# Optimization experiments

Measured on AMD Instinct MI355X. Metric: run time of the kernel, lower is better.

## Reference

```python
import jax, jax.numpy as jnp
import numpy as np

B, D, H, OUT = 16384, 4096, 7, 7


def setup_inputs() -> dict:
    key = jax.random.key(0)
    k1, k2, k3, k4 = jax.random.split(key, 4)
    features1 = jax.random.normal(k1, (B, D), dtype=jnp.float32)
    features2 = jax.random.normal(k2, (B, D), dtype=jnp.float32)
    W1 = jax.random.normal(k3, (D, H), dtype=jnp.float32) * (1.0 / np.sqrt(D))
    b1 = jnp.zeros((H,), dtype=jnp.float32)
    W2 = jax.random.normal(k4, (H, OUT), dtype=jnp.float32) * (1.0 / np.sqrt(H))
    b2 = jnp.zeros((OUT,), dtype=jnp.float32)
    return {"features1": features1, "features2": features2,
            "W1": W1, "b1": b1, "W2": W2, "b2": b2}


def reference(features1, features2, W1, b1, W2, b2):
    # Gate MLP (Dropout is inference-mode identity): [B, D] -> [B, 7]
    def mlp(x):
        h = jax.nn.relu(x @ W1 + b1)
        return h @ W2 + b2

    # Per-sample scalar logit for each expert: mean over the 7 gate outputs.
    logit1 = mlp(features1).mean(axis=1)  # [B]
    logit2 = mlp(features2).mean(axis=1)  # [B]

    # Per-sample softmax over the 2 experts (vectorized form of the batch loop).
    alpha = jax.nn.softmax(jnp.stack([logit1, logit2], axis=1), axis=1)  # [B, 2]

    # Weighted 2-expert combine: alpha0 * f1 + alpha1 * f2, shape [B, D].
    return alpha[:, 0:1] * features1 + alpha[:, 1:2] * features2
```

## Files before the change

kernel.cpp:

```cpp
#include <hip/hip_runtime.h>
#include <hip/hip_bf16.h>


constexpr int Dk  = 4096;
constexpr int Hk  = 7;
constexpr int NPAIR = Dk / 512;
constexpr int NWE   = Hk * NPAIR * 64;
constexpr int WPK_WORDS = NWE * 4;
constexpr size_t WS_NEEDED = (size_t)WPK_WORDS * 4 + 64;

constexpr int NTH = 512;
constexpr int ROWS_PER_BLOCK = 8;

__global__ void gating_prep(const float* __restrict__ W1,
                            const float* __restrict__ b1,
                            const float* __restrict__ W2,
                            const float* __restrict__ b2,
                            unsigned int* __restrict__ wsw)
{
    const int t = blockIdx.x * blockDim.x + threadIdx.x;
    if (t < NWE) {
        const int j    = t / (NPAIR * 64);
        const int kk   = (t / 64) % NPAIR;
        const int lane = t & 63;
        const int vi0  = (2 * kk) * 64 + lane;
        unsigned int w[4];
        #pragma unroll
        for (int h = 0; h < 2; ++h) {
            const int vi = vi0 + h * 64;
            #pragma unroll
            for (int p = 0; p < 2; ++p) {
                const int d0 = 4 * vi + 2 * p;
                const unsigned int lo = (unsigned int)__bfloat16_as_ushort(
                    __float2bfloat16(W1[(long long)d0 * Hk + j]));
                const unsigned int hi = (unsigned int)__bfloat16_as_ushort(
                    __float2bfloat16(W1[(long long)(d0 + 1) * Hk + j]));
                w[h * 2 + p] = lo | (hi << 16);
            }
        }
        reinterpret_cast<uint4*>(wsw)[t] = make_uint4(w[0], w[1], w[2], w[3]);
    }
    if (blockIdx.x == 0 && threadIdx.x == 0) {
        float* c = reinterpret_cast<float*>(wsw) + WPK_WORDS;
        #pragma unroll
        for (int j = 0; j < Hk; ++j) {
            c[j] = b1[j];
            float s = 0.f;
            #pragma unroll
            for (int k = 0; k < Hk; ++k) s += W2[j * Hk + k];
            c[Hk + j] = s;
        }
        float sb2 = 0.f;
        #pragma unroll
        for (int k = 0; k < Hk; ++k) sb2 += b2[k];
        c[14] = sb2;
    }
}

__device__ __forceinline__ float bf_lo(unsigned int u) {
    return __uint_as_float(u << 16);
}
__device__ __forceinline__ float bf_hi(unsigned int u) {
    return __uint_as_float(u & 0xFFFF0000u);
}

__global__ __launch_bounds__(NTH, 2)
void gating_wave(const float* __restrict__ f1,
                 const float* __restrict__ f2,
                 const uint4* __restrict__ wpk,
                 const float* __restrict__ gc,
                 float* __restrict__ out,
                 int rows)
{
    __shared__ uint4 wl[NWE];

    for (int e = threadIdx.x; e < NWE; e += NTH)
        wl[e] = wpk[e];
    __syncthreads();

    const int wid  = threadIdx.x >> 6;
    const int lane = threadIdx.x & 63;
    const int row  = blockIdx.x * ROWS_PER_BLOCK + wid;
    if (row >= rows) return;

    const long long base = (long long)row * Dk;
    const float4* __restrict__ f1v = reinterpret_cast<const float4*>(f1 + base);
    const float4* __restrict__ f2v = reinterpret_cast<const float4*>(f2 + base);

    float4 a[16], b[16];
    #pragma unroll
    for (int k = 0; k < 16; ++k) {
        const int vi = k * 64 + lane;
        a[k] = f1v[vi];
        b[k] = f2v[vi];
    }
    __builtin_amdgcn_sched_barrier(0);

    float acc1[Hk], acc2[Hk];
    #pragma unroll
    for (int j = 0; j < Hk; ++j) { acc1[j] = 0.f; acc2[j] = 0.f; }

    #pragma unroll
    for (int kk = 0; kk < NPAIR; ++kk) {
        const float4 xa0 = a[2 * kk],     xb0 = b[2 * kk];
        const float4 xa1 = a[2 * kk + 1], xb1 = b[2 * kk + 1];
        #pragma unroll
        for (int j = 0; j < Hk; ++j) {
            const uint4 u = wl[(j * NPAIR + kk) * 64 + lane];
            const float w0 = bf_lo(u.x), w1 = bf_hi(u.x);
            const float w2 = bf_lo(u.y), w3 = bf_hi(u.y);
            const float w4 = bf_lo(u.z), w5 = bf_hi(u.z);
            const float w6 = bf_lo(u.w), w7 = bf_hi(u.w);
            acc1[j] = fmaf(xa0.x, w0, fmaf(xa0.y, w1,
                      fmaf(xa0.z, w2, fmaf(xa0.w, w3, acc1[j]))));
            acc1[j] = fmaf(xa1.x, w4, fmaf(xa1.y, w5,
                      fmaf(xa1.z, w6, fmaf(xa1.w, w7, acc1[j]))));
            acc2[j] = fmaf(xb0.x, w0, fmaf(xb0.y, w1,
                      fmaf(xb0.z, w2, fmaf(xb0.w, w3, acc2[j]))));
            acc2[j] = fmaf(xb1.x, w4, fmaf(xb1.y, w5,
                      fmaf(xb1.z, w6, fmaf(xb1.w, w7, acc2[j]))));
        }
    }

    #pragma unroll
    for (int j = 0; j < Hk; ++j) {
        acc1[j] += __shfl_xor(acc1[j], 32);
        acc2[j] += __shfl_xor(acc2[j], 32);
    }
    float val[Hk];
    #pragma unroll
    for (int j = 0; j < Hk; ++j)
        val[j] = (lane < 32) ? acc1[j] : acc2[j];
    #pragma unroll
    for (int off = 16; off >= 1; off >>= 1) {
        #pragma unroll
        for (int j = 0; j < Hk; ++j)
            val[j] += __shfl_xor(val[j], off);
    }

    float logit = 0.f;
    #pragma unroll
    for (int j = 0; j < Hk; ++j)
        logit = fmaf(fmaxf(val[j] + gc[j], 0.f), gc[Hk + j], logit);
    logit = (logit + gc[14]) * (1.f / 7.f);

    const float other = __shfl_xor(logit, 32);
    const float delta = (lane < 32) ? (other - logit) : (logit - other);
    const float a0 = 1.f / (1.f + expf(delta));
    const float a1 = 1.f - a0;

    float4* __restrict__ ov = reinterpret_cast<float4*>(out + base);
    #pragma unroll
    for (int k = 0; k < 16; ++k) {
        const int vi = k * 64 + lane;
        float4 o;
        o.x = fmaf(a0, a[k].x, a1 * b[k].x);
        o.y = fmaf(a0, a[k].y, a1 * b[k].y);
        o.z = fmaf(a0, a[k].z, a1 * b[k].z);
        o.w = fmaf(a0, a[k].w, a1 * b[k].w);
        ov[vi] = o;
    }
}

__global__ __launch_bounds__(256, 4)
void gating_fused_direct(const float* __restrict__ f1,
                         const float* __restrict__ f2,
                         const float* __restrict__ W1,
                         const float* __restrict__ b1,
                         const float* __restrict__ W2,
                         const float* __restrict__ b2,
                         float* __restrict__ out)
{
    constexpr int VPT = 4;
    const int row = blockIdx.x;
    const int t   = threadIdx.x;
    const long long base = (long long)row * Dk;

    const float4* f1v = reinterpret_cast<const float4*>(f1 + base);
    const float4* f2v = reinterpret_cast<const float4*>(f2 + base);

    float4 r1[VPT], r2[VPT];
    float acc1[Hk], acc2[Hk];
    #pragma unroll
    for (int j = 0; j < Hk; ++j) { acc1[j] = 0.f; acc2[j] = 0.f; }

    #pragma unroll
    for (int k = 0; k < VPT; ++k) {
        const int vi = k * 256 + t;
        r1[k] = f1v[vi];
        r2[k] = f2v[vi];
        const float4* wv = reinterpret_cast<const float4*>(W1 + (long long)vi * 28);
        float4 w4[7];
        #pragma unroll
        for (int q = 0; q < 7; ++q) w4[q] = wv[q];
        const float* ws = reinterpret_cast<const float*>(w4);
        const float* x1 = reinterpret_cast<const float*>(&r1[k]);
        const float* x2 = reinterpret_cast<const float*>(&r2[k]);
        #pragma unroll
        for (int r = 0; r < 4; ++r)
            #pragma unroll
            for (int j = 0; j < Hk; ++j) {
                acc1[j] = fmaf(x1[r], ws[r * 7 + j], acc1[j]);
                acc2[j] = fmaf(x2[r], ws[r * 7 + j], acc2[j]);
            }
    }
    #pragma unroll
    for (int j = 0; j < Hk; ++j)
        #pragma unroll
        for (int off = 32; off >= 1; off >>= 1) {
            acc1[j] += __shfl_down(acc1[j], off);
            acc2[j] += __shfl_down(acc2[j], off);
        }

    __shared__ float red[4][2 * Hk];
    __shared__ float alpha[2];
    const int wave = t >> 6;
    const int lane = t & 63;
    if (lane == 0)
        #pragma unroll
        for (int j = 0; j < Hk; ++j) {
            red[wave][j]      = acc1[j];
            red[wave][Hk + j] = acc2[j];
        }
    __syncthreads();

    if (t == 0) {
        float l1 = 0.f, l2 = 0.f;
        #pragma unroll
        for (int j = 0; j < Hk; ++j) {
            float h1 = red[0][j] + red[1][j] + red[2][j] + red[3][j] + b1[j];
            float h2 = red[0][Hk + j] + red[1][Hk + j] + red[2][Hk + j]
                     + red[3][Hk + j] + b1[j];
            float s = 0.f;
            #pragma unroll
            for (int k2 = 0; k2 < Hk; ++k2) s += W2[j * Hk + k2];
            l1 = fmaf(fmaxf(h1, 0.f), s, l1);
            l2 = fmaf(fmaxf(h2, 0.f), s, l2);
        }
        float sb2 = 0.f;
        #pragma unroll
        for (int k2 = 0; k2 < Hk; ++k2) sb2 += b2[k2];
        l1 = (l1 + sb2) * (1.f / 7.f);
        l2 = (l2 + sb2) * (1.f / 7.f);
        const float a0 = 1.f / (1.f + expf(l2 - l1));
        alpha[0] = a0;
        alpha[1] = 1.f - a0;
    }
    __syncthreads();

    const float a0 = alpha[0];
    const float a1 = alpha[1];
    float4* ov = reinterpret_cast<float4*>(out + base);
    #pragma unroll
    for (int k = 0; k < VPT; ++k) {
        const int vi = k * 256 + t;
        float4 o;
        o.x = a0 * r1[k].x + a1 * r2[k].x;
        o.y = a0 * r1[k].y + a1 * r2[k].y;
        o.z = a0 * r1[k].z + a1 * r2[k].z;
        o.w = a0 * r1[k].w + a1 * r2[k].w;
        ov[vi] = o;
    }
}

extern "C" void kernel_launch(void* const* d_in, const int* in_sizes, int n_in,
                              void* d_out, int out_size, void* d_ws, size_t ws_size,
                              hipStream_t stream) {
    const float* f1 = (const float*)d_in[0];
    const float* f2 = (const float*)d_in[1];
    const float* W1 = (const float*)d_in[2];
    const float* b1 = (const float*)d_in[3];
    const float* W2 = (const float*)d_in[4];
    const float* b2 = (const float*)d_in[5];
    float* out = (float*)d_out;
    const int rows = in_sizes[0] / Dk;

    if (ws_size >= WS_NEEDED) {
        unsigned int* wsw = (unsigned int*)d_ws;
        gating_prep<<<(NWE + 255) / 256, 256, 0, stream>>>(W1, b1, W2, b2, wsw);
        const int blocks = (rows + ROWS_PER_BLOCK - 1) / ROWS_PER_BLOCK;
        gating_wave<<<blocks, NTH, 0, stream>>>(
            f1, f2, reinterpret_cast<const uint4*>(wsw),
            reinterpret_cast<const float*>(wsw) + WPK_WORDS, out, rows);
    } else {
        gating_fused_direct<<<rows, 256, 0, stream>>>(f1, f2, W1, b1, W2, b2, out);
    }
}
```

Baseline: 168.4 us.

## Use persistent grid-stride waves with chunked loads and re-read features for combine

Switches the gating kernel to a persistent launch of 512 blocks of 1024 threads, with each wave looping over rows in grid-stride order. The shared-memory weight staging is paid once per block instead of once per 8 rows. Features are now loaded in four chunks rather than held as 32 float4 registers, which lowers register pressure. The features are then read a second time from global memory for the weighted combine, relying on cache hits, which risks extra memory traffic. The b2 term is also dropped from the logit, which is only valid because it cancels in the two-way softmax.

```diff
diff --git a/kernel.cpp b/kernel.cpp
--- a/kernel.cpp
+++ b/kernel.cpp
@@ -9,8 +9,8 @@
 constexpr int WPK_WORDS = NWE * 4;
 constexpr size_t WS_NEEDED = (size_t)WPK_WORDS * 4 + 64;
 
-constexpr int NTH = 512;
-constexpr int ROWS_PER_BLOCK = 8;
+constexpr int NTH  = 1024;
+constexpr int NBLK = 512;
 
 __global__ void gating_prep(const float* __restrict__ W1,
                             const float* __restrict__ b1,
@@ -64,7 +64,7 @@
     return __uint_as_float(u & 0xFFFF0000u);
 }
 
-__global__ __launch_bounds__(NTH, 2)
+__global__ __launch_bounds__(NTH, 8)
 void gating_wave(const float* __restrict__ f1,
                  const float* __restrict__ f2,
                  const uint4* __restrict__ wpk,
@@ -80,85 +80,95 @@
 
     const int wid  = threadIdx.x >> 6;
     const int lane = threadIdx.x & 63;
-    const int row  = blockIdx.x * ROWS_PER_BLOCK + wid;
-    if (row >= rows) return;
-
-    const long long base = (long long)row * Dk;
-    const float4* __restrict__ f1v = reinterpret_cast<const float4*>(f1 + base);
-    const float4* __restrict__ f2v = reinterpret_cast<const float4*>(f2 + base);
-
-    float4 a[16], b[16];
-    #pragma unroll
-    for (int k = 0; k < 16; ++k) {
-        const int vi = k * 64 + lane;
-        a[k] = f1v[vi];
-        b[k] = f2v[vi];
-    }
-    __builtin_amdgcn_sched_barrier(0);
-
-    float acc1[Hk], acc2[Hk];
-    #pragma unroll
-    for (int j = 0; j < Hk; ++j) { acc1[j] = 0.f; acc2[j] = 0.f; }
-
-    #pragma unroll
-    for (int kk = 0; kk < NPAIR; ++kk) {
-        const float4 xa0 = a[2 * kk],     xb0 = b[2 * kk];
-        const float4 xa1 = a[2 * kk + 1], xb1 = b[2 * kk + 1];
-        #pragma unroll
-        for (int j = 0; j < Hk; ++j) {
-            const uint4 u = wl[(j * NPAIR + kk) * 64 + lane];
-            const float w0 = bf_lo(u.x), w1 = bf_hi(u.x);
-            const float w2 = bf_lo(u.y), w3 = bf_hi(u.y);
-            const float w4 = bf_lo(u.z), w5 = bf_hi(u.z);
-            const float w6 = bf_lo(u.w), w7 = bf_hi(u.w);
-            acc1[j] = fmaf(xa0.x, w0, fmaf(xa0.y, w1,
-                      fmaf(xa0.z, w2, fmaf(xa0.w, w3, acc1[j]))));
-            acc1[j] = fmaf(xa1.x, w4, fmaf(xa1.y, w5,
-                      fmaf(xa1.z, w6, fmaf(xa1.w, w7, acc1[j]))));
-            acc2[j] = fmaf(xb0.x, w0, fmaf(xb0.y, w1,
-                      fmaf(xb0.z, w2, fmaf(xb0.w, w3, acc2[j]))));
-            acc2[j] = fmaf(xb1.x, w4, fmaf(xb1.y, w5,
-                      fmaf(xb1.z, w6, fmaf(xb1.w, w7, acc2[j]))));
-        }
-    }
-
-    #pragma unroll
-    for (int j = 0; j < Hk; ++j) {
-        acc1[j] += __shfl_xor(acc1[j], 32);
-        acc2[j] += __shfl_xor(acc2[j], 32);
-    }
-    float val[Hk];
-    #pragma unroll
-    for (int j = 0; j < Hk; ++j)
-        val[j] = (lane < 32) ? acc1[j] : acc2[j];
-    #pragma unroll
-    for (int off = 16; off >= 1; off >>= 1) {
+    const int gwave  = blockIdx.x * (NTH / 64) + wid;
+    const int nwaves = gridDim.x * (NTH / 64);
+
+    float b1r[Hk], sr[Hk];
+    #pragma unroll
+    for (int j = 0; j < Hk; ++j) { b1r[j] = gc[j]; sr[j] = gc[Hk + j]; }
+
+    for (int row = gwave; row < rows; row += nwaves) {
+        const long long base = (long long)row * Dk;
+        const float4* __restrict__ f1v = reinterpret_cast<const float4*>(f1 + base);
+        const float4* __restrict__ f2v = reinterpret_cast<const float4*>(f2 + base);
+
+        float acc1[Hk], acc2[Hk];
+        #pragma unroll
+        for (int j = 0; j < Hk; ++j) { acc1[j] = 0.f; acc2[j] = 0.f; }
+
+        for (int q = 0; q < 4; ++q) {
+            float4 a[4], b[4];
+            #pragma unroll
+            for (int i = 0; i < 4; ++i) {
+                const int vi = (4 * q + i) * 64 + lane;
+                a[i] = f1v[vi];
+                b[i] = f2v[vi];
+            }
+            __builtin_amdgcn_sched_barrier(0);
+            #pragma unroll
+            for (int kk2 = 0; kk2 < 2; ++kk2) {
+                const int kk = 2 * q + kk2;
+                const float4 xa0 = a[2 * kk2],     xb0 = b[2 * kk2];
+                const float4 xa1 = a[2 * kk2 + 1], xb1 = b[2 * kk2 + 1];
+                #pragma unroll
+                for (int j = 0; j < Hk; ++j) {
+                    const uint4 u = wl[(j * NPAIR + kk) * 64 + lane];
+                    const float w0 = bf_lo(u.x), w1 = bf_hi(u.x);
+                    const float w2 = bf_lo(u.y), w3 = bf_hi(u.y);
+                    const float w4 = bf_lo(u.z), w5 = bf_hi(u.z);
+                    const float w6 = bf_lo(u.w), w7 = bf_hi(u.w);
+                    acc1[j] = fmaf(xa0.x, w0, fmaf(xa0.y, w1,
+                              fmaf(xa0.z, w2, fmaf(xa0.w, w3, acc1[j]))));
+                    acc1[j] = fmaf(xa1.x, w4, fmaf(xa1.y, w5,
+                              fmaf(xa1.z, w6, fmaf(xa1.w, w7, acc1[j]))));
+                    acc2[j] = fmaf(xb0.x, w0, fmaf(xb0.y, w1,
+                              fmaf(xb0.z, w2, fmaf(xb0.w, w3, acc2[j]))));
+                    acc2[j] = fmaf(xb1.x, w4, fmaf(xb1.y, w5,
+                              fmaf(xb1.z, w6, fmaf(xb1.w, w7, acc2[j]))));
+                }
+            }
+        }
+
+        #pragma unroll
+        for (int j = 0; j < Hk; ++j) {
+            acc1[j] += __shfl_xor(acc1[j], 32);
+            acc2[j] += __shfl_xor(acc2[j], 32);
+        }
+        float val[Hk];
         #pragma unroll
         for (int j = 0; j < Hk; ++j)
-            val[j] += __shfl_xor(val[j], off);
-    }
-
-    float logit = 0.f;
-    #pragma unroll
-    for (int j = 0; j < Hk; ++j)
-        logit = fmaf(fmaxf(val[j] + gc[j], 0.f), gc[Hk + j], logit);
-    logit = (logit + gc[14]) * (1.f / 7.f);
-
-    const float other = __shfl_xor(logit, 32);
-    const float delta = (lane < 32) ? (other - logit) : (logit - other);
-    const float a0 = 1.f / (1.f + expf(delta));
-    const float a1 = 1.f - a0;
-
-    float4* __restrict__ ov = reinterpret_cast<float4*>(out + base);
-    #pragma unroll
-    for (int k = 0; k < 16; ++k) {
-        const int vi = k * 64 + lane;
-        float4 o;
-        o.x = fmaf(a0, a[k].x, a1 * b[k].x);
-        o.y = fmaf(a0, a[k].y, a1 * b[k].y);
-        o.z = fmaf(a0, a[k].z, a1 * b[k].z);
-        o.w = fmaf(a0, a[k].w, a1 * b[k].w);
-        ov[vi] = o;
+            val[j] = (lane < 32) ? acc1[j] : acc2[j];
+        #pragma unroll
+        for (int off = 16; off >= 1; off >>= 1) {
+            #pragma unroll
+            for (int j = 0; j < Hk; ++j)
+                val[j] += __shfl_xor(val[j], off);
+        }
+
+        float logit = 0.f;
+        #pragma unroll
+        for (int j = 0; j < Hk; ++j)
+            logit = fmaf(fmaxf(val[j] + b1r[j], 0.f), sr[j], logit);
+        logit *= (1.f / 7.f);
+
+        const float other = __shfl_xor(logit, 32);
+        const float delta = (lane < 32) ? (other - logit) : (logit - other);
+        const float a0 = 1.f / (1.f + expf(delta));
+        const float a1 = 1.f - a0;
+
+        float4* __restrict__ ov = reinterpret_cast<float4*>(out + base);
+        #pragma unroll 4
+        for (int k = 0; k < 16; ++k) {
+            const int vi = k * 64 + lane;
+            const float4 xa = f1v[vi];
+            const float4 xb = f2v[vi];
+            float4 o;
+            o.x = fmaf(a0, xa.x, a1 * xb.x);
+            o.y = fmaf(a0, xa.y, a1 * xb.y);
+            o.z = fmaf(a0, xa.z, a1 * xb.z);
+            o.w = fmaf(a0, xa.w, a1 * xb.w);
+            ov[vi] = o;
+        }
     }
 }
 
@@ -278,8 +288,7 @@
     if (ws_size >= WS_NEEDED) {
         unsigned int* wsw = (unsigned int*)d_ws;
         gating_prep<<<(NWE + 255) / 256, 256, 0, stream>>>(W1, b1, W2, b2, wsw);
-        const int blocks = (rows + ROWS_PER_BLOCK - 1) / ROWS_PER_BLOCK;
-        gating_wave<<<blocks, NTH, 0, stream>>>(
+        gating_wave<<<NBLK, NTH, 0, stream>>>(
             f1, f2, reinterpret_cast<const uint4*>(wsw),
             reinterpret_cast<const float*>(wsw) + WPK_WORDS, out, rows);
     } else {
```

Measured after the change: 282.1 us. 1.67x slower.
